# Kernel optimization log

Hardware: AMD Instinct MI355X
Metric: run time of the kernel (lower is better)

The kernel has to match this reference:

```python
import jax, jax.numpy as jnp
import numpy as np

N_P, N_A = 200_000, 100_000
D_P, D_A, H, OUT = 64, 64, 32, 1
E_PP, E_AP, E_PA = 3_200_000, 1_600_000, 1_600_000


def _lin(key, din, dout, bias=True):
    kw, kb = jax.random.split(key)
    W = jax.random.normal(kw, (din, dout), jnp.float32) * (1.0 / np.sqrt(din))
    if bias:
        b = jax.random.normal(kb, (dout,), jnp.float32) * 0.01
        return W, b
    return W


def setup_inputs() -> dict:
    key = jax.random.key(0)
    ks = jax.random.split(key, 24)
    inp = {}
    inp['x_paper'] = jax.random.normal(ks[0], (N_P, D_P), jnp.float32)
    inp['x_author'] = jax.random.normal(ks[1], (N_A, D_A), jnp.float32)
    inp['src_pp'] = jax.random.randint(ks[2], (E_PP,), 0, N_P)
    inp['dst_pp'] = jax.random.randint(ks[3], (E_PP,), 0, N_P)
    inp['src_ap'] = jax.random.randint(ks[4], (E_AP,), 0, N_A)
    inp['dst_ap'] = jax.random.randint(ks[5], (E_AP,), 0, N_P)
    inp['src_pa'] = jax.random.randint(ks[6], (E_PA,), 0, N_P)
    inp['dst_pa'] = jax.random.randint(ks[7], (E_PA,), 0, N_A)
    # Layer-1 SAGEConv weights per relation: lin_l (neighbor, with bias), lin_r (root, no bias)
    inp['Wl1_pp'], inp['bl1_pp'] = _lin(ks[8], D_P, H)
    inp['Wr1_pp'] = _lin(ks[9], D_P, H, bias=False)
    inp['Wl1_ap'], inp['bl1_ap'] = _lin(ks[10], D_A, H)
    inp['Wr1_ap'] = _lin(ks[11], D_P, H, bias=False)
    inp['Wl1_pa'], inp['bl1_pa'] = _lin(ks[12], D_P, H)
    inp['Wr1_pa'] = _lin(ks[13], D_A, H, bias=False)
    # Layer-2 SAGEConv weights (only relations feeding 'paper' affect the output)
    inp['Wl2_pp'], inp['bl2_pp'] = _lin(ks[14], H, H)
    inp['Wr2_pp'] = _lin(ks[15], H, H, bias=False)
    inp['Wl2_ap'], inp['bl2_ap'] = _lin(ks[16], H, H)
    inp['Wr2_ap'] = _lin(ks[17], H, H, bias=False)
    # Final classifier Linear(32, 1)
    inp['W_lin'], inp['b_lin'] = _lin(ks[18], H, OUT)
    return inp


def _sage_rel(x_src, x_dst, src, dst, Wl, bl, Wr):
    # SAGEConv: lin_l(mean_{j in N(i)} x_j) + lin_r(x_i)
    n_dst = x_dst.shape[0]
    agg = jax.ops.segment_sum(x_src[src], dst, num_segments=n_dst)
    cnt = jax.ops.segment_sum(jnp.ones((src.shape[0],), x_src.dtype), dst, num_segments=n_dst)
    mean = agg / jnp.maximum(cnt, 1.0)[:, None]
    return mean @ Wl + bl + x_dst @ Wr


def reference(x_paper, x_author, src_pp, dst_pp, src_ap, dst_ap, src_pa, dst_pa,
              Wl1_pp, bl1_pp, Wr1_pp, Wl1_ap, bl1_ap, Wr1_ap, Wl1_pa, bl1_pa, Wr1_pa,
              Wl2_pp, bl2_pp, Wr2_pp, Wl2_ap, bl2_ap, Wr2_ap, W_lin, b_lin):
    # Layer 1 (to_hetero: sum per-relation conv outputs per destination type), then relu
    p1 = (_sage_rel(x_paper, x_paper, src_pp, dst_pp, Wl1_pp, bl1_pp, Wr1_pp)
          + _sage_rel(x_author, x_paper, src_ap, dst_ap, Wl1_ap, bl1_ap, Wr1_ap))
    a1 = _sage_rel(x_paper, x_author, src_pa, dst_pa, Wl1_pa, bl1_pa, Wr1_pa)
    p1, a1 = jax.nn.relu(p1), jax.nn.relu(a1)
    # Layer 2: only 'paper' output is consumed downstream
    p2 = (_sage_rel(p1, p1, src_pp, dst_pp, Wl2_pp, bl2_pp, Wr2_pp)
          + _sage_rel(a1, p1, src_ap, dst_ap, Wl2_ap, bl2_ap, Wr2_ap))
    # model_config is None -> plain Linear, no sigmoid/softmax
    return p2 @ W_lin + b_lin
```

## Files before the change

kernel.cpp:

```cpp
#include <hip/hip_runtime.h>


typedef unsigned short ushort_t;
typedef __attribute__((ext_vector_type(8))) short bf16x8;
typedef __attribute__((ext_vector_type(4))) float f32x4;

#define PWBITS 9
#define PWIN   (1 << PWBITS)
#define PCHUNK 4096
#define CAPPAD 2048
#define FW_R   12

__device__ inline ushort_t f2bf(float f) {
    unsigned u = __float_as_uint(f);
    unsigned r = (u + 0x7FFFu + ((u >> 16) & 1u)) >> 16;
    return (ushort_t)r;
}
__device__ inline float bf2f_lo(unsigned u) { return __uint_as_float(u << 16); }
__device__ inline float bf2f_hi(unsigned u) { return __uint_as_float(u & 0xFFFF0000u); }
__device__ inline int ntl(const int* p) { return __builtin_nontemporal_load(p); }

__global__ void prep_weights(
    const float* __restrict__ Wl1_pp, const float* __restrict__ Wr1_pp,
    const float* __restrict__ Wl1_ap, const float* __restrict__ Wr1_ap,
    const float* __restrict__ Wl1_pa, const float* __restrict__ Wr1_pa,
    const float* __restrict__ bl1_pp, const float* __restrict__ bl1_ap,
    const float* __restrict__ bl1_pa,
    const float* __restrict__ Wl2_pp, const float* __restrict__ bl2_pp,
    const float* __restrict__ Wr2_pp,
    const float* __restrict__ Wl2_ap, const float* __restrict__ bl2_ap,
    const float* __restrict__ Wr2_ap,
    const float* __restrict__ W_lin, const float* __restrict__ b_lin,
    float* __restrict__ Wcomb_p, float* __restrict__ Wcomb_a,
    ushort_t* __restrict__ Wfrag_p, ushort_t* __restrict__ Wfrag_a,
    float* __restrict__ bias_p, float* __restrict__ bias_a,
    float* __restrict__ vv)
{
    int t = threadIdx.x;
    for (int idx = t; idx < 64 * 96; idx += 256) {
        int i = idx / 96, j = idx % 96;
        float v;
        if (j < 32)       v = Wl1_pp[i * 32 + j];
        else if (j < 64)  v = Wl1_pa[i * 32 + (j - 32)];
        else              v = Wr1_pp[i * 32 + (j - 64)] + Wr1_ap[i * 32 + (j - 64)];
        Wcomb_p[idx] = v;
    }
    for (int idx = t; idx < 64 * 64; idx += 256) {
        int i = idx / 64, j = idx % 64;
        Wcomb_a[idx] = (j < 32) ? Wl1_ap[i * 32 + j] : Wr1_pa[i * 32 + (j - 32)];
    }
    if (t < 32) {
        bias_p[t] = bl1_pp[t] + bl1_ap[t];
        bias_a[t] = bl1_pa[t];
        float vpp = 0.f, vr = 0.f, vap = 0.f;
        for (int j = 0; j < 32; ++j) {
            float wl = W_lin[j];
            vpp += Wl2_pp[t * 32 + j] * wl;
            vr  += (Wr2_pp[t * 32 + j] + Wr2_ap[t * 32 + j]) * wl;
            vap += Wl2_ap[t * 32 + j] * wl;
        }
        vv[t] = vpp; vv[32 + t] = vr; vv[96 + t] = vap;
    }
    if (t == 0) {
        float c = b_lin[0];
        for (int j = 0; j < 32; ++j) c += (bl2_pp[j] + bl2_ap[j]) * W_lin[j];
        vv[64] = c;
    }
    __syncthreads();
    for (int idx = t; idx < 12 * 64 * 8; idx += 256) {
        int f = idx >> 9, l = (idx >> 3) & 63, j = idx & 7;
        int nt = f >> 1, kh = f & 1;
        int k = kh * 32 + 8 * (l >> 4) + j;
        int n = nt * 16 + (l & 15);
        Wfrag_p[idx] = f2bf(Wcomb_p[k * 96 + n]);
    }
    for (int idx = t; idx < 8 * 64 * 8; idx += 256) {
        int f = idx >> 9, l = (idx >> 3) & 63, j = idx & 7;
        int nt = f >> 1, kh = f & 1;
        int k = kh * 32 + 8 * (l >> 4) + j;
        int n = nt * 16 + (l & 15);
        Wfrag_a[idx] = f2bf(Wcomb_a[k * 64 + n]);
    }
}

__global__ __launch_bounds__(256)
void partition3(
    const int* __restrict__ src0, const int* __restrict__ dst0, int E0,
    unsigned* __restrict__ bk0, int cap0, int nw0, int* __restrict__ wc0,
    const int* __restrict__ src1, const int* __restrict__ dst1, int E1,
    unsigned* __restrict__ bk1, int cap1, int nw1, int* __restrict__ wc1,
    const int* __restrict__ src2, const int* __restrict__ dst2, int E2,
    unsigned* __restrict__ bk2, int cap2, int nw2, int* __restrict__ wc2)
{
    __shared__ int lcnt[PWIN];
    __shared__ int lbase[PWIN];
    int nb0 = (E0 + PCHUNK - 1) / PCHUNK;
    int nb1 = (E1 + PCHUNK - 1) / PCHUNK;
    int b = blockIdx.x;
    const int* src; const int* dst; int E; unsigned* bk; int cap; int nw; int* wc; int chunk;
    if (b < nb0)            { src = src0; dst = dst0; E = E0; bk = bk0; cap = cap0; nw = nw0; wc = wc0; chunk = b; }
    else if (b < nb0 + nb1) { src = src1; dst = dst1; E = E1; bk = bk1; cap = cap1; nw = nw1; wc = wc1; chunk = b - nb0; }
    else                    { src = src2; dst = dst2; E = E2; bk = bk2; cap = cap2; nw = nw2; wc = wc2; chunk = b - nb0 - nb1; }
    int e0 = chunk * PCHUNK;
    int d_[16], s_[16];
#pragma unroll
    for (int r = 0; r < 4; ++r) {
        int base = e0 + r * 1024 + threadIdx.x * 4;
        if (base + 3 < E) {
            int4 dv = *(const int4*)(dst + base);
            int4 sv = *(const int4*)(src + base);
            d_[r * 4 + 0] = dv.x; d_[r * 4 + 1] = dv.y; d_[r * 4 + 2] = dv.z; d_[r * 4 + 3] = dv.w;
            s_[r * 4 + 0] = sv.x; s_[r * 4 + 1] = sv.y; s_[r * 4 + 2] = sv.z; s_[r * 4 + 3] = sv.w;
        } else {
#pragma unroll
            for (int k = 0; k < 4; ++k) {
                int e = base + k;
                d_[r * 4 + k] = (e < E) ? dst[e] : -1;
                s_[r * 4 + k] = 0;
            }
        }
    }
    for (int i = threadIdx.x; i < nw; i += 256) lcnt[i] = 0;
    __syncthreads();
#pragma unroll
    for (int k = 0; k < 16; ++k)
        if (d_[k] >= 0) atomicAdd(&lcnt[((unsigned)d_[k]) >> PWBITS], 1);
    __syncthreads();
    for (int i = threadIdx.x; i < nw; i += 256) {
        int c = lcnt[i];
        lbase[i] = (c > 0) ? atomicAdd(&wc[i * 16], c) : 0;
        lcnt[i] = 0;
    }
    __syncthreads();
#pragma unroll
    for (int k = 0; k < 16; ++k) {
        int d = d_[k];
        if (d >= 0) {
            int w = ((unsigned)d) >> PWBITS;
            int off = lbase[w] + atomicAdd(&lcnt[w], 1);
            if (off < cap)
                bk[(size_t)w * cap + off] =
                    (((unsigned)(d & (PWIN - 1))) << 18) | (unsigned)s_[k];
        }
    }
}

__device__ inline void fill_body(
    int b, const unsigned* __restrict__ bk, const int* __restrict__ wc, int cap,
    int* __restrict__ csr, int* __restrict__ cnt, int* __restrict__ rs,
    int N, int w, int* lc, int* wsum, int* wpre)
{
    int d0 = w << PWBITS;
    int sz = wc[w * 16]; if (sz > cap) sz = cap;
    const unsigned* bkt = bk + (size_t)w * cap;
    uint4 u[FW_R];
#pragma unroll
    for (int r = 0; r < FW_R; ++r) {
        int i4 = r * 1024 + threadIdx.x * 4;
        if (i4 + 3 < sz) {
            u[r] = *(const uint4*)(bkt + i4);
        } else {
            u[r].x = (i4 + 0 < sz) ? bkt[i4 + 0] : 0xFFFFFFFFu;
            u[r].y = (i4 + 1 < sz) ? bkt[i4 + 1] : 0xFFFFFFFFu;
            u[r].z = (i4 + 2 < sz) ? bkt[i4 + 2] : 0xFFFFFFFFu;
            u[r].w = (i4 + 3 < sz) ? bkt[i4 + 3] : 0xFFFFFFFFu;
        }
    }
    for (int i = threadIdx.x; i < PWIN; i += 256) lc[i] = 0;
    __syncthreads();
#pragma unroll
    for (int r = 0; r < FW_R; ++r) {
        if (u[r].x != 0xFFFFFFFFu) atomicAdd(&lc[u[r].x >> 18], 1);
        if (u[r].y != 0xFFFFFFFFu) atomicAdd(&lc[u[r].y >> 18], 1);
        if (u[r].z != 0xFFFFFFFFu) atomicAdd(&lc[u[r].z >> 18], 1);
        if (u[r].w != 0xFFFFFFFFu) atomicAdd(&lc[u[r].w >> 18], 1);
    }
    __syncthreads();
    {
        int i = threadIdx.x * 2;
        int d = d0 + i;
        if (d < N)     cnt[d] = lc[i];
        if (d + 1 < N) cnt[d + 1] = lc[i + 1];
    }
    int t2 = threadIdx.x * 2;
    int v0 = lc[t2], v1 = lc[t2 + 1];
    int ts = v0 + v1;
    int lane = threadIdx.x & 63;
    int wid = threadIdx.x >> 6;
    int incl = ts;
#pragma unroll
    for (int off = 1; off < 64; off <<= 1) {
        int o = __shfl_up(incl, off);
        if (lane >= off) incl += o;
    }
    if (lane == 63) wsum[wid] = incl;
    __syncthreads();
    if (threadIdx.x == 0) {
        int r = 0;
        for (int i = 0; i < 4; ++i) { wpre[i] = r; r += wsum[i]; }
    }
    __syncthreads();
    int run = w * cap + wpre[wid] + (incl - ts);
    lc[t2] = run;
    if (d0 + t2 < N) rs[d0 + t2] = run;
    run += v0;
    lc[t2 + 1] = run;
    if (d0 + t2 + 1 < N) rs[d0 + t2 + 1] = run;
    __syncthreads();
#pragma unroll
    for (int r = 0; r < FW_R; ++r) {
        if (u[r].x != 0xFFFFFFFFu) { int p = atomicAdd(&lc[u[r].x >> 18], 1); csr[p] = (int)(u[r].x & 0x3FFFFu); }
        if (u[r].y != 0xFFFFFFFFu) { int p = atomicAdd(&lc[u[r].y >> 18], 1); csr[p] = (int)(u[r].y & 0x3FFFFu); }
        if (u[r].z != 0xFFFFFFFFu) { int p = atomicAdd(&lc[u[r].z >> 18], 1); csr[p] = (int)(u[r].z & 0x3FFFFu); }
        if (u[r].w != 0xFFFFFFFFu) { int p = atomicAdd(&lc[u[r].w >> 18], 1); csr[p] = (int)(u[r].w & 0x3FFFFu); }
    }
}

__device__ inline bf16x8 cvt8(const float* p) {
    float4 a = *(const float4*)p;
    float4 b = *(const float4*)(p + 4);
    bf16x8 r;
    r[0] = (short)f2bf(a.x); r[1] = (short)f2bf(a.y);
    r[2] = (short)f2bf(a.z); r[3] = (short)f2bf(a.w);
    r[4] = (short)f2bf(b.x); r[5] = (short)f2bf(b.y);
    r[6] = (short)f2bf(b.z); r[7] = (short)f2bf(b.w);
    return r;
}

__device__ inline void proj_paper_body(
    int blk, const float* __restrict__ x, const ushort_t* __restrict__ Wfrag,
    const float* __restrict__ bias,
    ushort_t* __restrict__ h_pp, ushort_t* __restrict__ h_pa,
    float* __restrict__ root_p, int N)
{
    int wave = threadIdx.x >> 6, lane = threadIdx.x & 63;
    int mbase = blk * 64 + wave * 16;
    int row = lane & 15, grp = lane >> 4;
    int nA = mbase + row; if (nA > N - 1) nA = N - 1;
    const float* xr = x + (size_t)nA * 64 + grp * 8;
    bf16x8 a0 = cvt8(xr);
    bf16x8 a1 = cvt8(xr + 32);
    f32x4 acc0 = {0.f, 0.f, 0.f, 0.f}, acc1 = acc0, acc2 = acc0, acc3 = acc0;
    float bp0 = bias[row];
    float bp1 = bias[16 + row];
    f32x4 acc4 = {bp0, bp0, bp0, bp0};
    f32x4 acc5 = {bp1, bp1, bp1, bp1};
    const bf16x8* wf = (const bf16x8*)(Wfrag) + lane;
    acc0 = __builtin_amdgcn_mfma_f32_16x16x32_bf16(a0, wf[0 * 64], acc0, 0, 0, 0);
    acc0 = __builtin_amdgcn_mfma_f32_16x16x32_bf16(a1, wf[1 * 64], acc0, 0, 0, 0);
    acc1 = __builtin_amdgcn_mfma_f32_16x16x32_bf16(a0, wf[2 * 64], acc1, 0, 0, 0);
    acc1 = __builtin_amdgcn_mfma_f32_16x16x32_bf16(a1, wf[3 * 64], acc1, 0, 0, 0);
    acc2 = __builtin_amdgcn_mfma_f32_16x16x32_bf16(a0, wf[4 * 64], acc2, 0, 0, 0);
    acc2 = __builtin_amdgcn_mfma_f32_16x16x32_bf16(a1, wf[5 * 64], acc2, 0, 0, 0);
    acc3 = __builtin_amdgcn_mfma_f32_16x16x32_bf16(a0, wf[6 * 64], acc3, 0, 0, 0);
    acc3 = __builtin_amdgcn_mfma_f32_16x16x32_bf16(a1, wf[7 * 64], acc3, 0, 0, 0);
    acc4 = __builtin_amdgcn_mfma_f32_16x16x32_bf16(a0, wf[8 * 64], acc4, 0, 0, 0);
    acc4 = __builtin_amdgcn_mfma_f32_16x16x32_bf16(a1, wf[9 * 64], acc4, 0, 0, 0);
    acc5 = __builtin_amdgcn_mfma_f32_16x16x32_bf16(a0, wf[10 * 64], acc5, 0, 0, 0);
    acc5 = __builtin_amdgcn_mfma_f32_16x16x32_bf16(a1, wf[11 * 64], acc5, 0, 0, 0);
    int node0 = mbase + grp * 4;
#pragma unroll
    for (int reg = 0; reg < 4; ++reg) {
        int nd = node0 + reg;
        if (nd < N) {
            size_t b32 = (size_t)nd * 32;
            h_pp[b32 + row]        = f2bf(acc0[reg]);
            h_pp[b32 + 16 + row]   = f2bf(acc1[reg]);
            h_pa[b32 + row]        = f2bf(acc2[reg]);
            h_pa[b32 + 16 + row]   = f2bf(acc3[reg]);
            root_p[b32 + row]      = acc4[reg];
            root_p[b32 + 16 + row] = acc5[reg];
        }
    }
}

__device__ inline void proj_author_body(
    int blk, const float* __restrict__ x, const ushort_t* __restrict__ Wfrag,
    const float* __restrict__ bias,
    ushort_t* __restrict__ h_ap, float* __restrict__ root_a, int N)
{
    int wave = threadIdx.x >> 6, lane = threadIdx.x & 63;
    int mbase = blk * 64 + wave * 16;
    int row = lane & 15, grp = lane >> 4;
    int nA = mbase + row; if (nA > N - 1) nA = N - 1;
    const float* xr = x + (size_t)nA * 64 + grp * 8;
    bf16x8 a0 = cvt8(xr);
    bf16x8 a1 = cvt8(xr + 32);
    f32x4 acc0 = {0.f, 0.f, 0.f, 0.f}, acc1 = acc0;
    float bp0 = bias[row];
    float bp1 = bias[16 + row];
    f32x4 acc2 = {bp0, bp0, bp0, bp0};
    f32x4 acc3 = {bp1, bp1, bp1, bp1};
    const bf16x8* wf = (const bf16x8*)(Wfrag) + lane;
    acc0 = __builtin_amdgcn_mfma_f32_16x16x32_bf16(a0, wf[0 * 64], acc0, 0, 0, 0);
    acc0 = __builtin_amdgcn_mfma_f32_16x16x32_bf16(a1, wf[1 * 64], acc0, 0, 0, 0);
    acc1 = __builtin_amdgcn_mfma_f32_16x16x32_bf16(a0, wf[2 * 64], acc1, 0, 0, 0);
    acc1 = __builtin_amdgcn_mfma_f32_16x16x32_bf16(a1, wf[3 * 64], acc1, 0, 0, 0);
    acc2 = __builtin_amdgcn_mfma_f32_16x16x32_bf16(a0, wf[4 * 64], acc2, 0, 0, 0);
    acc2 = __builtin_amdgcn_mfma_f32_16x16x32_bf16(a1, wf[5 * 64], acc2, 0, 0, 0);
    acc3 = __builtin_amdgcn_mfma_f32_16x16x32_bf16(a0, wf[6 * 64], acc3, 0, 0, 0);
    acc3 = __builtin_amdgcn_mfma_f32_16x16x32_bf16(a1, wf[7 * 64], acc3, 0, 0, 0);
    int node0 = mbase + grp * 4;
#pragma unroll
    for (int reg = 0; reg < 4; ++reg) {
        int nd = node0 + reg;
        if (nd < N) {
            size_t b32 = (size_t)nd * 32;
            h_ap[b32 + row]        = f2bf(acc0[reg]);
            h_ap[b32 + 16 + row]   = f2bf(acc1[reg]);
            root_a[b32 + row]      = acc2[reg];
            root_a[b32 + 16 + row] = acc3[reg];
        }
    }
}

__global__ __launch_bounds__(256)
void fill_proj(
    const unsigned* __restrict__ bk0, const int* __restrict__ wc0, int cap0,
    int* __restrict__ csr0, int* __restrict__ cnt0, int* __restrict__ rs0, int N0, int nw0,
    const unsigned* __restrict__ bk1, const int* __restrict__ wc1, int cap1,
    int* __restrict__ csr1, int* __restrict__ cnt1, int* __restrict__ rs1, int N1, int nw1,
    const unsigned* __restrict__ bk2, const int* __restrict__ wc2, int cap2,
    int* __restrict__ csr2, int* __restrict__ cnt2, int* __restrict__ rs2, int N2, int nw2,
    const float* __restrict__ xp, const float* __restrict__ xa,
    const ushort_t* __restrict__ Wfp, const ushort_t* __restrict__ Wfa,
    const float* __restrict__ bias_p, const float* __restrict__ bias_a,
    ushort_t* __restrict__ h_pp, ushort_t* __restrict__ h_pa,
    ushort_t* __restrict__ h_ap,
    float* __restrict__ root_p, float* __restrict__ root_a,
    int NP, int NA, int pbp)
{
    __shared__ int lc[PWIN];
    __shared__ int wsum[4], wpre[4];
    int b = blockIdx.x;
    int nwt = nw0 + nw1 + nw2;
    if (b < nwt) {
        const unsigned* bk; const int* wc; int cap; int* csr; int* cnt; int* rs; int N; int w;
        if (b < nw0)            { bk = bk0; wc = wc0; cap = cap0; csr = csr0; cnt = cnt0; rs = rs0; N = N0; w = b; }
        else if (b < nw0 + nw1) { bk = bk1; wc = wc1; cap = cap1; csr = csr1; cnt = cnt1; rs = rs1; N = N1; w = b - nw0; }
        else                    { bk = bk2; wc = wc2; cap = cap2; csr = csr2; cnt = cnt2; rs = rs2; N = N2; w = b - nw0 - nw1; }
        fill_body(b, bk, wc, cap, csr, cnt, rs, N, w, lc, wsum, wpre);
    } else if (b < nwt + pbp) {
        proj_paper_body(b - nwt, xp, Wfp, bias_p, h_pp, h_pa, root_p, NP);
    } else {
        proj_author_body(b - nwt - pbp, xa, Wfa, bias_a, h_ap, root_a, NA);
    }
}

#define ACC8(A, U) \
    A[0] += bf2f_lo((U).x); A[1] += bf2f_hi((U).x); \
    A[2] += bf2f_lo((U).y); A[3] += bf2f_hi((U).y); \
    A[4] += bf2f_lo((U).z); A[5] += bf2f_hi((U).z); \
    A[6] += bf2f_lo((U).w); A[7] += bf2f_hi((U).w);

__global__ __launch_bounds__(256, 8)
void pull_paper(const ushort_t* __restrict__ h_pp, const ushort_t* __restrict__ h_ap,
                const float* __restrict__ root,
                const int* __restrict__ csr_pp, const int* __restrict__ rs_pp,
                const int* __restrict__ cnt_pp,
                const int* __restrict__ csr_ap, const int* __restrict__ rs_ap,
                const int* __restrict__ cnt_ap,
                const float* __restrict__ vv,
                float* __restrict__ s_pp, float* __restrict__ out, int N)
{
    __shared__ float v0[32], v1[32];
    __shared__ float c2s;
    if (threadIdx.x < 32) { v0[threadIdx.x] = vv[threadIdx.x]; v1[threadIdx.x] = vv[32 + threadIdx.x]; }
    if (threadIdx.x == 0) c2s = vv[64];
    __syncthreads();
    int n = blockIdx.x * 64 + (threadIdx.x >> 2);
    if (n >= N) return;
    int c = threadIdx.x & 3;
    float a[8];
#pragma unroll
    for (int k = 0; k < 8; ++k) a[k] = 0.f;
    int s1 = rs_pp[n], k1 = cnt_pp[n], e1 = s1 + k1;
    int j = s1;
    for (; j + 4 <= e1; j += 4) {
        int i0 = ntl(csr_pp + j), i1 = ntl(csr_pp + j + 1);
        int i2 = ntl(csr_pp + j + 2), i3 = ntl(csr_pp + j + 3);
        uint4 u0 = ((const uint4*)(h_pp + (size_t)i0 * 32))[c];
        uint4 u1 = ((const uint4*)(h_pp + (size_t)i1 * 32))[c];
        uint4 u2 = ((const uint4*)(h_pp + (size_t)i2 * 32))[c];
        uint4 u3 = ((const uint4*)(h_pp + (size_t)i3 * 32))[c];
        ACC8(a, u0) ACC8(a, u1) ACC8(a, u2) ACC8(a, u3)
    }
    for (; j < e1; ++j) {
        uint4 u0 = ((const uint4*)(h_pp + (size_t)ntl(csr_pp + j) * 32))[c];
        ACC8(a, u0)
    }
    float b[8];
#pragma unroll
    for (int k = 0; k < 8; ++k) b[k] = 0.f;
    int s2 = rs_ap[n], k2 = cnt_ap[n], e2 = s2 + k2;
    j = s2;
    for (; j + 4 <= e2; j += 4) {
        int i0 = ntl(csr_ap + j), i1 = ntl(csr_ap + j + 1);
        int i2 = ntl(csr_ap + j + 2), i3 = ntl(csr_ap + j + 3);
        uint4 u0 = ((const uint4*)(h_ap + (size_t)i0 * 32))[c];
        uint4 u1 = ((const uint4*)(h_ap + (size_t)i1 * 32))[c];
        uint4 u2 = ((const uint4*)(h_ap + (size_t)i2 * 32))[c];
        uint4 u3 = ((const uint4*)(h_ap + (size_t)i3 * 32))[c];
        ACC8(b, u0) ACC8(b, u1) ACC8(b, u2) ACC8(b, u3)
    }
    for (; j < e2; ++j) {
        uint4 u0 = ((const uint4*)(h_ap + (size_t)ntl(csr_ap + j) * 32))[c];
        ACC8(b, u0)
    }
    float ipp = 1.0f / fmaxf((float)k1, 1.0f);
    float iap = 1.0f / fmaxf((float)k2, 1.0f);
    const float* rt = root + (size_t)n * 32 + 8 * c;
    float d0 = 0.f, d1 = 0.f;
#pragma unroll
    for (int k = 0; k < 8; ++k) {
        float p = fmaxf(rt[k] + a[k] * ipp + b[k] * iap, 0.f);
        d0 += p * v0[8 * c + k];
        d1 += p * v1[8 * c + k];
    }
    d0 += __shfl_xor(d0, 1); d0 += __shfl_xor(d0, 2);
    d1 += __shfl_xor(d1, 1); d1 += __shfl_xor(d1, 2);
    if (c == 0) { s_pp[n] = d0; out[n] = d1 + c2s; }
}

__global__ __launch_bounds__(256, 8)
void pull_author(const ushort_t* __restrict__ h_pa, const float* __restrict__ root,
                 const int* __restrict__ csr_pa, const int* __restrict__ rs_pa,
                 const int* __restrict__ cnt_pa,
                 const float* __restrict__ vv, float* __restrict__ s_ap, int N)
{
    __shared__ float v0[32];
    if (threadIdx.x < 32) v0[threadIdx.x] = vv[96 + threadIdx.x];
    __syncthreads();
    int n = blockIdx.x * 64 + (threadIdx.x >> 2);
    if (n >= N) return;
    int c = threadIdx.x & 3;
    float a[8];
#pragma unroll
    for (int k = 0; k < 8; ++k) a[k] = 0.f;
    int s1 = rs_pa[n], k1 = cnt_pa[n], e1 = s1 + k1;
    int j = s1;
    for (; j + 4 <= e1; j += 4) {
        int i0 = ntl(csr_pa + j), i1 = ntl(csr_pa + j + 1);
        int i2 = ntl(csr_pa + j + 2), i3 = ntl(csr_pa + j + 3);
        uint4 u0 = ((const uint4*)(h_pa + (size_t)i0 * 32))[c];
        uint4 u1 = ((const uint4*)(h_pa + (size_t)i1 * 32))[c];
        uint4 u2 = ((const uint4*)(h_pa + (size_t)i2 * 32))[c];
        uint4 u3 = ((const uint4*)(h_pa + (size_t)i3 * 32))[c];
        ACC8(a, u0) ACC8(a, u1) ACC8(a, u2) ACC8(a, u3)
    }
    for (; j < e1; ++j) {
        uint4 u0 = ((const uint4*)(h_pa + (size_t)ntl(csr_pa + j) * 32))[c];
        ACC8(a, u0)
    }
    float ip = 1.0f / fmaxf((float)k1, 1.0f);
    const float* rt = root + (size_t)n * 32 + 8 * c;
    float d0 = 0.f;
#pragma unroll
    for (int k = 0; k < 8; ++k) {
        float p = fmaxf(rt[k] + a[k] * ip, 0.f);
        d0 += p * v0[8 * c + k];
    }
    d0 += __shfl_xor(d0, 1); d0 += __shfl_xor(d0, 2);
    if (c == 0) s_ap[n] = d0;
}

__global__ __launch_bounds__(256, 8)
void pull2(const float* __restrict__ s_pp, const float* __restrict__ s_ap,
           const int* __restrict__ csr_pp, const int* __restrict__ rs_pp,
           const int* __restrict__ cnt_pp,
           const int* __restrict__ csr_ap, const int* __restrict__ rs_ap,
           const int* __restrict__ cnt_ap,
           float* __restrict__ out, int N)
{
    int g = (blockIdx.x * blockDim.x + threadIdx.x) >> 2;
    int c = threadIdx.x & 3;
    if (g >= N) return;
    int s1 = rs_pp[g], k1 = cnt_pp[g], e1 = s1 + k1;
    float t = 0.f;
    for (int j = s1 + c; j < e1; j += 4) t += s_pp[ntl(csr_pp + j)];
    int s2 = rs_ap[g], k2 = cnt_ap[g], e2 = s2 + k2;
    float u = 0.f;
    for (int j = s2 + c; j < e2; j += 4) u += s_ap[ntl(csr_ap + j)];
    t += __shfl_xor(t, 1); t += __shfl_xor(t, 2);
    u += __shfl_xor(u, 1); u += __shfl_xor(u, 2);
    if (c == 0) {
        out[g] += t / fmaxf((float)k1, 1.f) + u / fmaxf((float)k2, 1.f);
    }
}

extern "C" void kernel_launch(void* const* d_in, const int* in_sizes, int n_in,
                              void* d_out, int out_size, void* d_ws, size_t ws_size,
                              hipStream_t stream)
{
    const float* x_paper  = (const float*)d_in[0];
    const float* x_author = (const float*)d_in[1];
    const int* src_pp = (const int*)d_in[2];
    const int* dst_pp = (const int*)d_in[3];
    const int* src_ap = (const int*)d_in[4];
    const int* dst_ap = (const int*)d_in[5];
    const int* src_pa = (const int*)d_in[6];
    const int* dst_pa = (const int*)d_in[7];
    const float* Wl1_pp = (const float*)d_in[8];
    const float* bl1_pp = (const float*)d_in[9];
    const float* Wr1_pp = (const float*)d_in[10];
    const float* Wl1_ap = (const float*)d_in[11];
    const float* bl1_ap = (const float*)d_in[12];
    const float* Wr1_ap = (const float*)d_in[13];
    const float* Wl1_pa = (const float*)d_in[14];
    const float* bl1_pa = (const float*)d_in[15];
    const float* Wr1_pa = (const float*)d_in[16];
    const float* Wl2_pp = (const float*)d_in[17];
    const float* bl2_pp = (const float*)d_in[18];
    const float* Wr2_pp = (const float*)d_in[19];
    const float* Wl2_ap = (const float*)d_in[20];
    const float* bl2_ap = (const float*)d_in[21];
    const float* Wr2_ap = (const float*)d_in[22];
    const float* W_lin  = (const float*)d_in[23];
    const float* b_lin  = (const float*)d_in[24];

    const int NP = in_sizes[0] / 64;
    const int NA = in_sizes[1] / 64;
    const int E_PP = in_sizes[2];
    const int E_AP = in_sizes[4];
    const int E_PA = in_sizes[6];

    const int nw_pp = (NP + PWIN - 1) >> PWBITS;
    const int nw_ap = nw_pp;
    const int nw_pa = (NA + PWIN - 1) >> PWBITS;
    const int cap_pp = ((E_PP / nw_pp + CAPPAD) + 3) & ~3;
    const int cap_ap = ((E_AP / nw_ap + CAPPAD) + 3) & ~3;
    const int cap_pa = ((E_PA / nw_pa + CAPPAD) + 3) & ~3;

    char* wp = (char*)d_ws;
    int* wcur = (int*)wp;             wp += (size_t)3 * PWIN * 16 * 4;
    unsigned* bk_pp = (unsigned*)wp;  wp += (size_t)nw_pp * cap_pp * 4;
    unsigned* bk_ap = (unsigned*)wp;  wp += (size_t)nw_ap * cap_ap * 4;
    unsigned* bk_pa = (unsigned*)wp;  wp += (size_t)nw_pa * cap_pa * 4;
    int* csr_pp = (int*)wp;           wp += (size_t)nw_pp * cap_pp * 4;
    int* csr_ap = (int*)wp;           wp += (size_t)nw_ap * cap_ap * 4;
    int* csr_pa = (int*)wp;           wp += (size_t)nw_pa * cap_pa * 4;
    int* cnt    = (int*)wp;           wp += (size_t)(2 * NP + NA) * 4;
    int* rs     = (int*)wp;           wp += (size_t)(2 * NP + NA) * 4;
    ushort_t* h_pp = (ushort_t*)wp;   wp += (size_t)NP * 32 * 2;
    ushort_t* h_pa = (ushort_t*)wp;   wp += (size_t)NP * 32 * 2;
    ushort_t* h_ap = (ushort_t*)wp;   wp += (size_t)NA * 32 * 2;
    float* root_a = (float*)wp;       wp += (size_t)NA * 32 * 4;
    float* s_pp   = (float*)wp;       wp += (size_t)NP * 4;
    float* s_ap   = (float*)wp;       wp += (size_t)NA * 4;
    float* Wcomb_p = (float*)wp;      wp += 64 * 96 * 4;
    float* Wcomb_a = (float*)wp;      wp += 64 * 64 * 4;
    ushort_t* Wfrag_p = (ushort_t*)wp; wp += 12 * 64 * 8 * 2;
    ushort_t* Wfrag_a = (ushort_t*)wp; wp += 8 * 64 * 8 * 2;
    float* bias_p = (float*)wp;       wp += 32 * 4;
    float* bias_a = (float*)wp;       wp += 32 * 4;
    float* vv     = (float*)wp;       wp += 128 * 4;
    size_t used = (size_t)(wp - (char*)d_ws);
    size_t rootp_bytes = (size_t)NP * 32 * 4;
    bool roomy = (used + rootp_bytes) <= ws_size;
    float* root_p = roomy ? (float*)wp : (float*)bk_pp;

    int* cnt_pp = cnt,  * cnt_ap = cnt + NP,  * cnt_pa = cnt + 2 * NP;
    int* rs_pp  = rs,   * rs_ap  = rs + NP,   * rs_pa  = rs + 2 * NP;

    float* out = (float*)d_out;

    hipMemsetAsync(wcur, 0, (size_t)3 * PWIN * 16 * 4, stream);

    prep_weights<<<1, 256, 0, stream>>>(
        Wl1_pp, Wr1_pp, Wl1_ap, Wr1_ap, Wl1_pa, Wr1_pa,
        bl1_pp, bl1_ap, bl1_pa,
        Wl2_pp, bl2_pp, Wr2_pp, Wl2_ap, bl2_ap, Wr2_ap,
        W_lin, b_lin, Wcomb_p, Wcomb_a, Wfrag_p, Wfrag_a, bias_p, bias_a, vv);

    int nb_total = (E_PP + PCHUNK - 1) / PCHUNK + (E_AP + PCHUNK - 1) / PCHUNK
                 + (E_PA + PCHUNK - 1) / PCHUNK;
    int pbp = (NP + 63) / 64;
    int pba = (NA + 63) / 64;
    int nwt = nw_pp + nw_ap + nw_pa;

    partition3<<<nb_total, 256, 0, stream>>>(
        src_pp, dst_pp, E_PP, bk_pp, cap_pp, nw_pp, wcur + 0,
        src_ap, dst_ap, E_AP, bk_ap, cap_ap, nw_ap, wcur + PWIN * 16,
        src_pa, dst_pa, E_PA, bk_pa, cap_pa, nw_pa, wcur + 2 * PWIN * 16);

    if (roomy) {
        fill_proj<<<nwt + pbp + pba, 256, 0, stream>>>(
            bk_pp, wcur + 0,             cap_pp, csr_pp, cnt_pp, rs_pp, NP, nw_pp,
            bk_ap, wcur + PWIN * 16,     cap_ap, csr_ap, cnt_ap, rs_ap, NP, nw_ap,
            bk_pa, wcur + 2 * PWIN * 16, cap_pa, csr_pa, cnt_pa, rs_pa, NA, nw_pa,
            x_paper, x_author, Wfrag_p, Wfrag_a, bias_p, bias_a,
            h_pp, h_pa, h_ap, root_p, root_a, NP, NA, pbp);
    } else {
        fill_proj<<<nwt, 256, 0, stream>>>(
            bk_pp, wcur + 0,             cap_pp, csr_pp, cnt_pp, rs_pp, NP, nw_pp,
            bk_ap, wcur + PWIN * 16,     cap_ap, csr_ap, cnt_ap, rs_ap, NP, nw_ap,
            bk_pa, wcur + 2 * PWIN * 16, cap_pa, csr_pa, cnt_pa, rs_pa, NA, nw_pa,
            x_paper, x_author, Wfrag_p, Wfrag_a, bias_p, bias_a,
            h_pp, h_pa, h_ap, root_p, root_a, NP, NA, 0x40000000);
        fill_proj<<<pbp + pba, 256, 0, stream>>>(
            bk_pp, wcur + 0,             cap_pp, csr_pp, cnt_pp, rs_pp, NP, 0,
            bk_ap, wcur + PWIN * 16,     cap_ap, csr_ap, cnt_ap, rs_ap, NP, 0,
            bk_pa, wcur + 2 * PWIN * 16, cap_pa, csr_pa, cnt_pa, rs_pa, NA, 0,
            x_paper, x_author, Wfrag_p, Wfrag_a, bias_p, bias_a,
            h_pp, h_pa, h_ap, root_p, root_a, NP, NA, pbp);
    }

    pull_paper<<<(NP + 63) / 64, 256, 0, stream>>>(
        h_pp, h_ap, root_p, csr_pp, rs_pp, cnt_pp, csr_ap, rs_ap, cnt_ap,
        vv, s_pp, out, NP);
    pull_author<<<(NA + 63) / 64, 256, 0, stream>>>(
        h_pa, root_a, csr_pa, rs_pa, cnt_pa, vv, s_ap, NA);

    pull2<<<((size_t)NP * 4 + 255) / 256, 256, 0, stream>>>(
        s_pp, s_ap, csr_pp, rs_pp, cnt_pp, csr_ap, rs_ap, cnt_ap, out, NP);
}
```

Measured before the change: 373.7 us.

## Stage partitioned edges in LDS for coalesced bucket writes; merge pull kernels

The partition kernel now computes a block-local prefix sum over window counts and stages each chunk's packed edges in shared memory, sorted by window. It then writes them to the global buckets in contiguous runs instead of scattering each edge directly. Separately, the paper and author pull kernels are merged into one launch, with the blocks split by index. This is meant to make bucket writes coalesced and save a launch, at the cost of about 26KB more LDS per partition block, which can lower occupancy. The scan also hardcodes 512 windows per block, assuming nw is at most PWIN.

Measured after the change: 346.1 us. -7.4%, faster.

```diff
diff --git a/kernel.cpp b/kernel.cpp
--- a/kernel.cpp
+++ b/kernel.cpp
@@ -93,14 +93,18 @@
     unsigned* __restrict__ bk2, int cap2, int nw2, int* __restrict__ wc2)
 {
     __shared__ int lcnt[PWIN];
+    __shared__ int lsta[PWIN];
     __shared__ int lbase[PWIN];
+    __shared__ unsigned stg[PCHUNK];
+    __shared__ ushort_t wsl[PCHUNK];
+    __shared__ int wsum[4], wpre[4];
     int nb0 = (E0 + PCHUNK - 1) / PCHUNK;
     int nb1 = (E1 + PCHUNK - 1) / PCHUNK;
     int b = blockIdx.x;
-    const int* src; const int* dst; int E; unsigned* bk; int cap; int nw; int* wc; int chunk;
-    if (b < nb0)            { src = src0; dst = dst0; E = E0; bk = bk0; cap = cap0; nw = nw0; wc = wc0; chunk = b; }
-    else if (b < nb0 + nb1) { src = src1; dst = dst1; E = E1; bk = bk1; cap = cap1; nw = nw1; wc = wc1; chunk = b - nb0; }
-    else                    { src = src2; dst = dst2; E = E2; bk = bk2; cap = cap2; nw = nw2; wc = wc2; chunk = b - nb0 - nb1; }
+    const int* src; const int* dst; int E; unsigned* bk; int cap; int* wc; int chunk;
+    if (b < nb0)            { src = src0; dst = dst0; E = E0; bk = bk0; cap = cap0; wc = wc0; chunk = b; }
+    else if (b < nb0 + nb1) { src = src1; dst = dst1; E = E1; bk = bk1; cap = cap1; wc = wc1; chunk = b - nb0; }
+    else                    { src = src2; dst = dst2; E = E2; bk = bk2; cap = cap2; wc = wc2; chunk = b - nb0 - nb1; }
     int e0 = chunk * PCHUNK;
     int d_[16], s_[16];
 #pragma unroll
@@ -120,33 +124,61 @@
             }
         }
     }
-    for (int i = threadIdx.x; i < nw; i += 256) lcnt[i] = 0;
+    for (int i = threadIdx.x; i < PWIN; i += 256) lcnt[i] = 0;
     __syncthreads();
 #pragma unroll
     for (int k = 0; k < 16; ++k)
         if (d_[k] >= 0) atomicAdd(&lcnt[((unsigned)d_[k]) >> PWBITS], 1);
     __syncthreads();
-    for (int i = threadIdx.x; i < nw; i += 256) {
-        int c = lcnt[i];
-        lbase[i] = (c > 0) ? atomicAdd(&wc[i * 16], c) : 0;
-        lcnt[i] = 0;
-    }
+    int t2 = threadIdx.x * 2;
+    int v0 = lcnt[t2], v1 = lcnt[t2 + 1];
+    lbase[t2]     = (v0 > 0) ? atomicAdd(&wc[t2 * 16], v0) : 0;
+    lbase[t2 + 1] = (v1 > 0) ? atomicAdd(&wc[(t2 + 1) * 16], v1) : 0;
+    int ts = v0 + v1;
+    int lane = threadIdx.x & 63;
+    int wid = threadIdx.x >> 6;
+    int incl = ts;
+#pragma unroll
+    for (int off = 1; off < 64; off <<= 1) {
+        int o = __shfl_up(incl, off);
+        if (lane >= off) incl += o;
+    }
+    if (lane == 63) wsum[wid] = incl;
+    __syncthreads();
+    if (threadIdx.x == 0) {
+        int r = 0;
+        for (int i = 0; i < 4; ++i) { wpre[i] = r; r += wsum[i]; }
+    }
+    __syncthreads();
+    int run = wpre[wid] + (incl - ts);
+    lsta[t2] = run;
+    run += v0;
+    lsta[t2 + 1] = run;
+    __syncthreads();
+    lcnt[t2] = lsta[t2];
+    lcnt[t2 + 1] = lsta[t2 + 1];
     __syncthreads();
 #pragma unroll
     for (int k = 0; k < 16; ++k) {
         int d = d_[k];
         if (d >= 0) {
             int w = ((unsigned)d) >> PWBITS;
-            int off = lbase[w] + atomicAdd(&lcnt[w], 1);
-            if (off < cap)
-                bk[(size_t)w * cap + off] =
-                    (((unsigned)(d & (PWIN - 1))) << 18) | (unsigned)s_[k];
-        }
+            int pos = atomicAdd(&lcnt[w], 1);
+            stg[pos] = (((unsigned)(d & (PWIN - 1))) << 18) | (unsigned)s_[k];
+            wsl[pos] = (ushort_t)w;
+        }
+    }
+    __syncthreads();
+    int total = E - e0; if (total > PCHUNK) total = PCHUNK;
+    for (int slot = threadIdx.x; slot < total; slot += 256) {
+        int w = wsl[slot];
+        int off = lbase[w] + (slot - lsta[w]);
+        if (off < cap) bk[(size_t)w * cap + off] = stg[slot];
     }
 }
 
 __device__ inline void fill_body(
-    int b, const unsigned* __restrict__ bk, const int* __restrict__ wc, int cap,
+    const unsigned* __restrict__ bk, const int* __restrict__ wc, int cap,
     int* __restrict__ csr, int* __restrict__ cnt, int* __restrict__ rs,
     int N, int w, int* lc, int* wsum, int* wpre)
 {
@@ -339,7 +371,7 @@
         if (b < nw0)            { bk = bk0; wc = wc0; cap = cap0; csr = csr0; cnt = cnt0; rs = rs0; N = N0; w = b; }
         else if (b < nw0 + nw1) { bk = bk1; wc = wc1; cap = cap1; csr = csr1; cnt = cnt1; rs = rs1; N = N1; w = b - nw0; }
         else                    { bk = bk2; wc = wc2; cap = cap2; csr = csr2; cnt = cnt2; rs = rs2; N = N2; w = b - nw0 - nw1; }
-        fill_body(b, bk, wc, cap, csr, cnt, rs, N, w, lc, wsum, wpre);
+        fill_body(bk, wc, cap, csr, cnt, rs, N, w, lc, wsum, wpre);
     } else if (b < nwt + pbp) {
         proj_paper_body(b - nwt, xp, Wfp, bias_p, h_pp, h_pa, root_p, NP);
     } else {
@@ -354,114 +386,111 @@
     A[6] += bf2f_lo((U).w); A[7] += bf2f_hi((U).w);
 
 __global__ __launch_bounds__(256, 8)
-void pull_paper(const ushort_t* __restrict__ h_pp, const ushort_t* __restrict__ h_ap,
-                const float* __restrict__ root,
-                const int* __restrict__ csr_pp, const int* __restrict__ rs_pp,
-                const int* __restrict__ cnt_pp,
-                const int* __restrict__ csr_ap, const int* __restrict__ rs_ap,
-                const int* __restrict__ cnt_ap,
-                const float* __restrict__ vv,
-                float* __restrict__ s_pp, float* __restrict__ out, int N)
+void pull_pa(const ushort_t* __restrict__ h_pp, const ushort_t* __restrict__ h_ap,
+             const ushort_t* __restrict__ h_pa,
+             const float* __restrict__ root_p, const float* __restrict__ root_a,
+             const int* __restrict__ csr_pp, const int* __restrict__ rs_pp,
+             const int* __restrict__ cnt_pp,
+             const int* __restrict__ csr_ap, const int* __restrict__ rs_ap,
+             const int* __restrict__ cnt_ap,
+             const int* __restrict__ csr_pa, const int* __restrict__ rs_pa,
+             const int* __restrict__ cnt_pa,
+             const float* __restrict__ vv,
+             float* __restrict__ s_pp, float* __restrict__ s_ap,
+             float* __restrict__ out, int NP, int NA, int pbp)
 {
     __shared__ float v0[32], v1[32];
     __shared__ float c2s;
-    if (threadIdx.x < 32) { v0[threadIdx.x] = vv[threadIdx.x]; v1[threadIdx.x] = vv[32 + threadIdx.x]; }
-    if (threadIdx.x == 0) c2s = vv[64];
-    __syncthreads();
-    int n = blockIdx.x * 64 + (threadIdx.x >> 2);
-    if (n >= N) return;
     int c = threadIdx.x & 3;
-    float a[8];
-#pragma unroll
-    for (int k = 0; k < 8; ++k) a[k] = 0.f;
-    int s1 = rs_pp[n], k1 = cnt_pp[n], e1 = s1 + k1;
-    int j = s1;
-    for (; j + 4 <= e1; j += 4) {
-        int i0 = ntl(csr_pp + j), i1 = ntl(csr_pp + j + 1);
-        int i2 = ntl(csr_pp + j + 2), i3 = ntl(csr_pp + j + 3);
-        uint4 u0 = ((const uint4*)(h_pp + (size_t)i0 * 32))[c];
-        uint4 u1 = ((const uint4*)(h_pp + (size_t)i1 * 32))[c];
-        uint4 u2 = ((const uint4*)(h_pp + (size_t)i2 * 32))[c];
-        uint4 u3 = ((const uint4*)(h_pp + (size_t)i3 * 32))[c];
-        ACC8(a, u0) ACC8(a, u1) ACC8(a, u2) ACC8(a, u3)
-    }
-    for (; j < e1; ++j) {
-        uint4 u0 = ((const uint4*)(h_pp + (size_t)ntl(csr_pp + j) * 32))[c];
-        ACC8(a, u0)
-    }
-    float b[8];
-#pragma unroll
-    for (int k = 0; k < 8; ++k) b[k] = 0.f;
-    int s2 = rs_ap[n], k2 = cnt_ap[n], e2 = s2 + k2;
-    j = s2;
-    for (; j + 4 <= e2; j += 4) {
-        int i0 = ntl(csr_ap + j), i1 = ntl(csr_ap + j + 1);
-        int i2 = ntl(csr_ap + j + 2), i3 = ntl(csr_ap + j + 3);
-        uint4 u0 = ((const uint4*)(h_ap + (size_t)i0 * 32))[c];
-        uint4 u1 = ((const uint4*)(h_ap + (size_t)i1 * 32))[c];
-        uint4 u2 = ((const uint4*)(h_ap + (size_t)i2 * 32))[c];
-        uint4 u3 = ((const uint4*)(h_ap + (size_t)i3 * 32))[c];
-        ACC8(b, u0) ACC8(b, u1) ACC8(b, u2) ACC8(b, u3)
-    }
-    for (; j < e2; ++j) {
-        uint4 u0 = ((const uint4*)(h_ap + (size_t)ntl(csr_ap + j) * 32))[c];
-        ACC8(b, u0)
-    }
-    float ipp = 1.0f / fmaxf((float)k1, 1.0f);
-    float iap = 1.0f / fmaxf((float)k2, 1.0f);
-    const float* rt = root + (size_t)n * 32 + 8 * c;
-    float d0 = 0.f, d1 = 0.f;
-#pragma unroll
-    for (int k = 0; k < 8; ++k) {
-        float p = fmaxf(rt[k] + a[k] * ipp + b[k] * iap, 0.f);
-        d0 += p * v0[8 * c + k];
-        d1 += p * v1[8 * c + k];
-    }
-    d0 += __shfl_xor(d0, 1); d0 += __shfl_xor(d0, 2);
-    d1 += __shfl_xor(d1, 1); d1 += __shfl_xor(d1, 2);
-    if (c == 0) { s_pp[n] = d0; out[n] = d1 + c2s; }
-}
-
-__global__ __launch_bounds__(256, 8)
-void pull_author(const ushort_t* __restrict__ h_pa, const float* __restrict__ root,
-                 const int* __restrict__ csr_pa, const int* __restrict__ rs_pa,
-                 const int* __restrict__ cnt_pa,
-                 const float* __restrict__ vv, float* __restrict__ s_ap, int N)
-{
-    __shared__ float v0[32];
-    if (threadIdx.x < 32) v0[threadIdx.x] = vv[96 + threadIdx.x];
-    __syncthreads();
-    int n = blockIdx.x * 64 + (threadIdx.x >> 2);
-    if (n >= N) return;
-    int c = threadIdx.x & 3;
-    float a[8];
-#pragma unroll
-    for (int k = 0; k < 8; ++k) a[k] = 0.f;
-    int s1 = rs_pa[n], k1 = cnt_pa[n], e1 = s1 + k1;
-    int j = s1;
-    for (; j + 4 <= e1; j += 4) {
-        int i0 = ntl(csr_pa + j), i1 = ntl(csr_pa + j + 1);
-        int i2 = ntl(csr_pa + j + 2), i3 = ntl(csr_pa + j + 3);
-        uint4 u0 = ((const uint4*)(h_pa + (size_t)i0 * 32))[c];
-        uint4 u1 = ((const uint4*)(h_pa + (size_t)i1 * 32))[c];
-        uint4 u2 = ((const uint4*)(h_pa + (size_t)i2 * 32))[c];
-        uint4 u3 = ((const uint4*)(h_pa + (size_t)i3 * 32))[c];
-        ACC8(a, u0) ACC8(a, u1) ACC8(a, u2) ACC8(a, u3)
-    }
-    for (; j < e1; ++j) {
-        uint4 u0 = ((const uint4*)(h_pa + (size_t)ntl(csr_pa + j) * 32))[c];
-        ACC8(a, u0)
-    }
-    float ip = 1.0f / fmaxf((float)k1, 1.0f);
-    const float* rt = root + (size_t)n * 32 + 8 * c;
-    float d0 = 0.f;
-#pragma unroll
-    for (int k = 0; k < 8; ++k) {
-        float p = fmaxf(rt[k] + a[k] * ip, 0.f);
-        d0 += p * v0[8 * c + k];
-    }
-    d0 += __shfl_xor(d0, 1); d0 += __shfl_xor(d0, 2);
-    if (c == 0) s_ap[n] = d0;
+    if (blockIdx.x < pbp) {
+        if (threadIdx.x < 32) { v0[threadIdx.x] = vv[threadIdx.x]; v1[threadIdx.x] = vv[32 + threadIdx.x]; }
+        if (threadIdx.x == 0) c2s = vv[64];
+        __syncthreads();
+        int n = blockIdx.x * 64 + (threadIdx.x >> 2);
+        if (n >= NP) return;
+        float a[8];
+#pragma unroll
+        for (int k = 0; k < 8; ++k) a[k] = 0.f;
+        int s1 = rs_pp[n], k1 = cnt_pp[n], e1 = s1 + k1;
+        int j = s1;
+        for (; j + 4 <= e1; j += 4) {
+            int i0 = ntl(csr_pp + j), i1 = ntl(csr_pp + j + 1);
+            int i2 = ntl(csr_pp + j + 2), i3 = ntl(csr_pp + j + 3);
+            uint4 u0 = ((const uint4*)(h_pp + (size_t)i0 * 32))[c];
+            uint4 u1 = ((const uint4*)(h_pp + (size_t)i1 * 32))[c];
+            uint4 u2 = ((const uint4*)(h_pp + (size_t)i2 * 32))[c];
+            uint4 u3 = ((const uint4*)(h_pp + (size_t)i3 * 32))[c];
+            ACC8(a, u0) ACC8(a, u1) ACC8(a, u2) ACC8(a, u3)
+        }
+        for (; j < e1; ++j) {
+            uint4 u0 = ((const uint4*)(h_pp + (size_t)ntl(csr_pp + j) * 32))[c];
+            ACC8(a, u0)
+        }
+        float b8[8];
+#pragma unroll
+        for (int k = 0; k < 8; ++k) b8[k] = 0.f;
+        int s2 = rs_ap[n], k2 = cnt_ap[n], e2 = s2 + k2;
+        j = s2;
+        for (; j + 4 <= e2; j += 4) {
+            int i0 = ntl(csr_ap + j), i1 = ntl(csr_ap + j + 1);
+            int i2 = ntl(csr_ap + j + 2), i3 = ntl(csr_ap + j + 3);
+            uint4 u0 = ((const uint4*)(h_ap + (size_t)i0 * 32))[c];
+            uint4 u1 = ((const uint4*)(h_ap + (size_t)i1 * 32))[c];
+            uint4 u2 = ((const uint4*)(h_ap + (size_t)i2 * 32))[c];
+            uint4 u3 = ((const uint4*)(h_ap + (size_t)i3 * 32))[c];
+            ACC8(b8, u0) ACC8(b8, u1) ACC8(b8, u2) ACC8(b8, u3)
+        }
+        for (; j < e2; ++j) {
+            uint4 u0 = ((const uint4*)(h_ap + (size_t)ntl(csr_ap + j) * 32))[c];
+            ACC8(b8, u0)
+        }
+        float ipp = 1.0f / fmaxf((float)k1, 1.0f);
+        float iap = 1.0f / fmaxf((float)k2, 1.0f);
+        const float* rt = root_p + (size_t)n * 32 + 8 * c;
+        float d0 = 0.f, d1 = 0.f;
+#pragma unroll
+        for (int k = 0; k < 8; ++k) {
+            float p = fmaxf(rt[k] + a[k] * ipp + b8[k] * iap, 0.f);
+            d0 += p * v0[8 * c + k];
+            d1 += p * v1[8 * c + k];
+        }
+        d0 += __shfl_xor(d0, 1); d0 += __shfl_xor(d0, 2);
+        d1 += __shfl_xor(d1, 1); d1 += __shfl_xor(d1, 2);
+        if (c == 0) { s_pp[n] = d0; out[n] = d1 + c2s; }
+    } else {
+        if (threadIdx.x < 32) v0[threadIdx.x] = vv[96 + threadIdx.x];
+        __syncthreads();
+        int n = (blockIdx.x - pbp) * 64 + (threadIdx.x >> 2);
+        if (n >= NA) return;
+        float a[8];
+#pragma unroll
+        for (int k = 0; k < 8; ++k) a[k] = 0.f;
+        int s1 = rs_pa[n], k1 = cnt_pa[n], e1 = s1 + k1;
+        int j = s1;
+        for (; j + 4 <= e1; j += 4) {
+            int i0 = ntl(csr_pa + j), i1 = ntl(csr_pa + j + 1);
+            int i2 = ntl(csr_pa + j + 2), i3 = ntl(csr_pa + j + 3);
+            uint4 u0 = ((const uint4*)(h_pa + (size_t)i0 * 32))[c];
+            uint4 u1 = ((const uint4*)(h_pa + (size_t)i1 * 32))[c];
+            uint4 u2 = ((const uint4*)(h_pa + (size_t)i2 * 32))[c];
+            uint4 u3 = ((const uint4*)(h_pa + (size_t)i3 * 32))[c];
+            ACC8(a, u0) ACC8(a, u1) ACC8(a, u2) ACC8(a, u3)
+        }
+        for (; j < e1; ++j) {
+            uint4 u0 = ((const uint4*)(h_pa + (size_t)ntl(csr_pa + j) * 32))[c];
+            ACC8(a, u0)
+        }
+        float ip = 1.0f / fmaxf((float)k1, 1.0f);
+        const float* rt = root_a + (size_t)n * 32 + 8 * c;
+        float d0 = 0.f;
+#pragma unroll
+        for (int k = 0; k < 8; ++k) {
+            float p = fmaxf(rt[k] + a[k] * ip, 0.f);
+            d0 += p * v0[8 * c + k];
+        }
+        d0 += __shfl_xor(d0, 1); d0 += __shfl_xor(d0, 2);
+        if (c == 0) s_ap[n] = d0;
+    }
 }
 
 __global__ __launch_bounds__(256, 8)
@@ -605,11 +634,10 @@
             h_pp, h_pa, h_ap, root_p, root_a, NP, NA, pbp);
     }
 
-    pull_paper<<<(NP + 63) / 64, 256, 0, stream>>>(
-        h_pp, h_ap, root_p, csr_pp, rs_pp, cnt_pp, csr_ap, rs_ap, cnt_ap,
-        vv, s_pp, out, NP);
-    pull_author<<<(NA + 63) / 64, 256, 0, stream>>>(
-        h_pa, root_a, csr_pa, rs_pa, cnt_pa, vv, s_ap, NA);
+    pull_pa<<<pbp + pba, 256, 0, stream>>>(
+        h_pp, h_ap, h_pa, root_p, root_a,
+        csr_pp, rs_pp, cnt_pp, csr_ap, rs_ap, cnt_ap, csr_pa, rs_pa, cnt_pa,
+        vv, s_pp, s_ap, out, NP, NA, pbp);
 
     pull2<<<((size_t)NP * 4 + 255) / 256, 256, 0, stream>>>(
         s_pp, s_ap, csr_pp, rs_pp, cnt_pp, csr_ap, rs_ap, cnt_ap, out, NP);
```
